# Performance work log

Measured on AMD Instinct MI355X. Metric: run time of the kernel, lower is better.

## Reference

```python
import jax, jax.numpy as jnp
import numpy as np

K, M, N = 8, 1024, 1024  # bits, in_features, out_features (nf)
B_, S_ = 4, 2048

def setup_inputs() -> dict:
    key = jax.random.key(0)
    k1, k2, k3, k4 = jax.random.split(key, 4)
    x = jax.random.normal(k1, (B_, S_, M), dtype=jnp.float32)
    # per-bit +/-1 sign matrices, stored as float (module casts int8 -> x.dtype)
    binary = jnp.where(jax.random.normal(k2, (K, M, N)) > 0, 1.0, -1.0).astype(jnp.float32)
    # positive per-bit, per-output-channel scales (sup decomposition yields positives)
    scale = jax.random.uniform(k3, (K, 1, N), dtype=jnp.float32, minval=0.01, maxval=1.0)
    bias = jax.random.normal(k4, (N,), dtype=jnp.float32)
    return {"x": x, "binary": binary, "scale": scale, "bias": bias}

def reference(x, binary, scale, bias):
    size_out = x.shape[:-1] + (N,)
    x2 = x.reshape(-1, x.shape[-1])                 # [T, m]
    # k separate dense matmuls against +/-1 matrices: [k, T, n]
    xk = jnp.einsum('tm,kmn->ktn', x2, binary)
    out = jnp.sum(xk * scale, axis=0)               # per-bit scale then sum over bits
    out = out + bias
    return out.reshape(size_out)
```

## Files before the change

kernel.cpp:

```cpp
#include <hip/hip_runtime.h>
#include <cstdint>

#define TDIM 8192
#define MDIM 1024
#define NDIM 1024
#define KBITS 8
#define BK 64

typedef __bf16 bf16x8 __attribute__((ext_vector_type(8)));
typedef float f32x4 __attribute__((ext_vector_type(4)));

#define GAS(p) ((__attribute__((address_space(1))) void*)(uintptr_t)(p))
#define LAS(p) ((__attribute__((address_space(3))) void*)(uintptr_t)(p))

__device__ __forceinline__ unsigned short f2bf(float f) {
    union { float f; unsigned u; } v; v.f = f;
    unsigned r = v.u + 0x7fffu + ((v.u >> 16) & 1u);
    return (unsigned short)(r >> 16);
}

__global__ __launch_bounds__(256) void prep_kernel(const float* __restrict__ x,
                                                   unsigned short* __restrict__ xb,
                                                   const float* __restrict__ binary,
                                                   const float* __restrict__ scale,
                                                   unsigned short* __restrict__ wtr) {
    __shared__ float tile[32][33];
    const int tid = threadIdx.x;
    if (blockIdx.x >= 1024) {
        size_t idx = ((size_t)(blockIdx.x - 1024) * 256 + tid) * 8;
        float4 a = *(const float4*)(x + idx);
        float4 b = *(const float4*)(x + idx + 4);
        uint4 o;
        o.x = (unsigned)f2bf(a.x) | ((unsigned)f2bf(a.y) << 16);
        o.y = (unsigned)f2bf(a.z) | ((unsigned)f2bf(a.w) << 16);
        o.z = (unsigned)f2bf(b.x) | ((unsigned)f2bf(b.y) << 16);
        o.w = (unsigned)f2bf(b.z) | ((unsigned)f2bf(b.w) << 16);
        *(uint4*)(xb + idx) = o;
        return;
    }
    const int n0 = (blockIdx.x & 31) * 32;
    const int m0 = (blockIdx.x >> 5) * 32;
    const int r = tid >> 3;
    const int cn = (tid & 7) * 4;
    f32x4 acc = {0.f, 0.f, 0.f, 0.f};
#pragma unroll
    for (int k = 0; k < KBITS; ++k) {
        f32x4 v = *(const f32x4*)(binary + ((size_t)k * MDIM + m0 + r) * NDIM + n0 + cn);
        f32x4 s = *(const f32x4*)(scale + (size_t)k * NDIM + n0 + cn);
        acc += v * s;
    }
#pragma unroll
    for (int e = 0; e < 4; ++e) tile[cn + e][r] = acc[e];
    __syncthreads();
    const int rn = tid >> 3;
    const int cm = (tid & 7) * 4;
    ushort4 o4;
    o4.x = f2bf(tile[rn][cm + 0]);
    o4.y = f2bf(tile[rn][cm + 1]);
    o4.z = f2bf(tile[rn][cm + 2]);
    o4.w = f2bf(tile[rn][cm + 3]);
    *(ushort4*)(wtr + (size_t)(n0 + rn) * MDIM + m0 + cm) = o4;
}

__global__ __launch_bounds__(256) void gemm_kernel(const unsigned short* __restrict__ xb,
                                                   const unsigned short* __restrict__ wtr,
                                                   const float* __restrict__ bias,
                                                   float* __restrict__ out) {
    __shared__ __attribute__((aligned(16))) unsigned short sA[128 * BK];
    __shared__ __attribute__((aligned(16))) unsigned short sB[128 * BK];

    const int tid = threadIdx.x;
    const int lane = tid & 63;
    const int wv = tid >> 6;
    const int wrow = wv >> 1;
    const int wcol = wv & 1;
    const int lrow = lane & 15;
    const int q = lane >> 4;

    const int t0 = blockIdx.x * 128;
    const int n0 = blockIdx.y * 128;

    const unsigned short* srcA[4];
    const unsigned short* srcB[4];
    unsigned short* dstA[4];
    unsigned short* dstB[4];
#pragma unroll
    for (int j = 0; j < 4; ++j) {
        int s = tid + j * 256;
        int r = s >> 3;
        int g = (s & 7) ^ (r & 7);
        srcA[j] = xb + (size_t)(t0 + r) * MDIM + g * 8;
        srcB[j] = wtr + (size_t)(n0 + r) * MDIM + g * 8;
        dstA[j] = sA + s * 8;
        dstB[j] = sB + s * 8;
    }

    int a_off[2][4], b_off[2][4];
#pragma unroll
    for (int h = 0; h < 2; ++h)
#pragma unroll
        for (int i = 0; i < 4; ++i) {
            int m = wrow * 64 + i * 16 + lrow;
            a_off[h][i] = (m * 8 + ((h * 4 + q) ^ (m & 7))) * 8;
            int n = wcol * 64 + i * 16 + lrow;
            b_off[h][i] = (n * 8 + ((h * 4 + q) ^ (n & 7))) * 8;
        }

    f32x4 acc[4][4];
    const f32x4 zero = {0.f, 0.f, 0.f, 0.f};
#pragma unroll
    for (int i = 0; i < 4; ++i)
#pragma unroll
        for (int j = 0; j < 4; ++j) acc[i][j] = zero;

    for (int k0 = 0; k0 < MDIM; k0 += BK) {
#pragma unroll
        for (int j = 0; j < 4; ++j)
            __builtin_amdgcn_global_load_lds(GAS(srcA[j] + k0), LAS(dstA[j]), 16, 0, 0);
#pragma unroll
        for (int j = 0; j < 4; ++j)
            __builtin_amdgcn_global_load_lds(GAS(srcB[j] + k0), LAS(dstB[j]), 16, 0, 0);
        __syncthreads();

#pragma unroll
        for (int h = 0; h < 2; ++h) {
            bf16x8 af[4], bfr[4];
#pragma unroll
            for (int i = 0; i < 4; ++i) af[i] = *(const bf16x8*)(sA + a_off[h][i]);
#pragma unroll
            for (int i = 0; i < 4; ++i) bfr[i] = *(const bf16x8*)(sB + b_off[h][i]);
#pragma unroll
            for (int i = 0; i < 4; ++i)
#pragma unroll
                for (int j = 0; j < 4; ++j)
                    acc[i][j] = __builtin_amdgcn_mfma_f32_16x16x32_bf16(af[i], bfr[j],
                                                                        acc[i][j], 0, 0, 0);
        }
        __syncthreads();
    }

#pragma unroll
    for (int j = 0; j < 4; ++j) {
        const int n = n0 + wcol * 64 + j * 16 + lrow;
        const float bv = bias[n];
#pragma unroll
        for (int i = 0; i < 4; ++i) {
            const int tb = t0 + wrow * 64 + i * 16 + q * 4;
#pragma unroll
            for (int r = 0; r < 4; ++r) {
                out[(size_t)(tb + r) * NDIM + n] = acc[i][j][r] + bv;
            }
        }
    }
}

extern "C" void kernel_launch(void* const* d_in, const int* in_sizes, int n_in,
                              void* d_out, int out_size, void* d_ws, size_t ws_size,
                              hipStream_t stream) {
    const float* x      = (const float*)d_in[0];
    const float* binary = (const float*)d_in[1];
    const float* scale  = (const float*)d_in[2];
    const float* bias   = (const float*)d_in[3];
    float* out = (float*)d_out;

    unsigned short* xb  = (unsigned short*)d_ws;
    unsigned short* wtr = xb + (size_t)TDIM * MDIM;

    prep_kernel<<<1024 + 4096, 256, 0, stream>>>(x, xb, binary, scale, wtr);
    gemm_kernel<<<dim3(TDIM / 128, NDIM / 128), 256, 0, stream>>>(xb, wtr, bias, out);
}
```

Baseline: 126.0 us.

## Triple-buffer LDS with 256x128 tiles and 512-thread blocks in GEMM

The GEMM moves from a single-buffered 128x128 tile with two barriers per K step to a 256x128 tile computed by 8 waves. A three-stage LDS ring issues global-to-LDS loads two tiles ahead and uses explicit vmcnt waits plus a single barrier per iteration. MFMA sections are also raised to higher priority with s_setprio. The aim is to hide global load latency and raise reuse of B per block, at the cost of about 144KB of LDS per block, which can cap occupancy at one block per CU and leaves fewer blocks (256) to fill the GPU.

```diff
diff --git a/kernel.cpp b/kernel.cpp
--- a/kernel.cpp
+++ b/kernel.cpp
@@ -6,6 +6,9 @@
 #define NDIM 1024
 #define KBITS 8
 #define BK 64
+#define BT 256
+#define BN 128
+#define NTILES (MDIM / BK)
 
 typedef __bf16 bf16x8 __attribute__((ext_vector_type(8)));
 typedef float f32x4 __attribute__((ext_vector_type(4)));
@@ -62,37 +65,45 @@
     *(ushort4*)(wtr + (size_t)(n0 + rn) * MDIM + m0 + cm) = o4;
 }
 
-__global__ __launch_bounds__(256) void gemm_kernel(const unsigned short* __restrict__ xb,
-                                                   const unsigned short* __restrict__ wtr,
-                                                   const float* __restrict__ bias,
-                                                   float* __restrict__ out) {
-    __shared__ __attribute__((aligned(16))) unsigned short sA[128 * BK];
-    __shared__ __attribute__((aligned(16))) unsigned short sB[128 * BK];
+__global__ __launch_bounds__(512, 2) void gemm_kernel(const unsigned short* __restrict__ xb,
+                                                      const unsigned short* __restrict__ wtr,
+                                                      const float* __restrict__ bias,
+                                                      float* __restrict__ out) {
+    constexpr int ASZ = BT * BK;
+    constexpr int BSZ = BN * BK;
+    constexpr int BUF = ASZ + BSZ;
+    __shared__ __attribute__((aligned(16))) unsigned short lds[3 * BUF];
 
     const int tid = threadIdx.x;
     const int lane = tid & 63;
     const int wv = tid >> 6;
-    const int wrow = wv >> 1;
-    const int wcol = wv & 1;
+    const int wm = wv >> 1;
+    const int wn = wv & 1;
     const int lrow = lane & 15;
     const int q = lane >> 4;
 
-    const int t0 = blockIdx.x * 128;
-    const int n0 = blockIdx.y * 128;
+    const int t0 = blockIdx.x * BT;
+    const int n0 = blockIdx.y * BN;
 
     const unsigned short* srcA[4];
-    const unsigned short* srcB[4];
-    unsigned short* dstA[4];
-    unsigned short* dstB[4];
+    int dstA[4];
+    const unsigned short* srcB[2];
+    int dstB[2];
 #pragma unroll
     for (int j = 0; j < 4; ++j) {
-        int s = tid + j * 256;
+        int s = tid + j * 512;
         int r = s >> 3;
         int g = (s & 7) ^ (r & 7);
         srcA[j] = xb + (size_t)(t0 + r) * MDIM + g * 8;
+        dstA[j] = s * 8;
+    }
+#pragma unroll
+    for (int j = 0; j < 2; ++j) {
+        int s = tid + j * 512;
+        int r = s >> 3;
+        int g = (s & 7) ^ (r & 7);
         srcB[j] = wtr + (size_t)(n0 + r) * MDIM + g * 8;
-        dstA[j] = sA + s * 8;
-        dstB[j] = sB + s * 8;
+        dstB[j] = ASZ + s * 8;
     }
 
     int a_off[2][4], b_off[2][4];
@@ -100,10 +111,10 @@
     for (int h = 0; h < 2; ++h)
 #pragma unroll
         for (int i = 0; i < 4; ++i) {
-            int m = wrow * 64 + i * 16 + lrow;
+            int m = wm * 64 + i * 16 + lrow;
             a_off[h][i] = (m * 8 + ((h * 4 + q) ^ (m & 7))) * 8;
-            int n = wcol * 64 + i * 16 + lrow;
-            b_off[h][i] = (n * 8 + ((h * 4 + q) ^ (n & 7))) * 8;
+            int n = wn * 64 + i * 16 + lrow;
+            b_off[h][i] = ASZ + (n * 8 + ((h * 4 + q) ^ (n & 7))) * 8;
         }
 
     f32x4 acc[4][4];
@@ -113,39 +124,64 @@
 #pragma unroll
         for (int j = 0; j < 4; ++j) acc[i][j] = zero;
 
-    for (int k0 = 0; k0 < MDIM; k0 += BK) {
+    auto stage = [&](int bufsel, int t) {
+        unsigned short* bb = lds + bufsel * BUF;
+        const int k0 = t * BK;
 #pragma unroll
         for (int j = 0; j < 4; ++j)
-            __builtin_amdgcn_global_load_lds(GAS(srcA[j] + k0), LAS(dstA[j]), 16, 0, 0);
-#pragma unroll
-        for (int j = 0; j < 4; ++j)
-            __builtin_amdgcn_global_load_lds(GAS(srcB[j] + k0), LAS(dstB[j]), 16, 0, 0);
-        __syncthreads();
-
+            __builtin_amdgcn_global_load_lds(GAS(srcA[j] + k0), LAS(bb + dstA[j]), 16, 0, 0);
+#pragma unroll
+        for (int j = 0; j < 2; ++j)
+            __builtin_amdgcn_global_load_lds(GAS(srcB[j] + k0), LAS(bb + dstB[j]), 16, 0, 0);
+    };
+
+    stage(0, 0);
+    stage(1, 1);
+    asm volatile("s_waitcnt vmcnt(6)" ::: "memory");
+    __builtin_amdgcn_s_barrier();
+    __builtin_amdgcn_sched_barrier(0);
+
+#pragma unroll
+    for (int t = 0; t < NTILES; ++t) {
+        const int cur = t % 3;
+        if (t + 2 < NTILES) stage((t + 2) % 3, t + 2);
+
+        const unsigned short* base = lds + cur * BUF;
 #pragma unroll
         for (int h = 0; h < 2; ++h) {
             bf16x8 af[4], bfr[4];
 #pragma unroll
-            for (int i = 0; i < 4; ++i) af[i] = *(const bf16x8*)(sA + a_off[h][i]);
-#pragma unroll
-            for (int i = 0; i < 4; ++i) bfr[i] = *(const bf16x8*)(sB + b_off[h][i]);
+            for (int i = 0; i < 4; ++i) af[i] = *(const bf16x8*)(base + a_off[h][i]);
+#pragma unroll
+            for (int i = 0; i < 4; ++i) bfr[i] = *(const bf16x8*)(base + b_off[h][i]);
+            __builtin_amdgcn_s_setprio(1);
 #pragma unroll
             for (int i = 0; i < 4; ++i)
 #pragma unroll
                 for (int j = 0; j < 4; ++j)
                     acc[i][j] = __builtin_amdgcn_mfma_f32_16x16x32_bf16(af[i], bfr[j],
                                                                         acc[i][j], 0, 0, 0);
-        }
-        __syncthreads();
+            __builtin_amdgcn_s_setprio(0);
+        }
+
+        if (t + 1 < NTILES) {
+            if (t + 2 < NTILES) {
+                asm volatile("s_waitcnt vmcnt(6)" ::: "memory");
+            } else {
+                asm volatile("s_waitcnt vmcnt(0)" ::: "memory");
+            }
+            __builtin_amdgcn_s_barrier();
+            __builtin_amdgcn_sched_barrier(0);
+        }
     }
 
 #pragma unroll
     for (int j = 0; j < 4; ++j) {
-        const int n = n0 + wcol * 64 + j * 16 + lrow;
+        const int n = n0 + wn * 64 + j * 16 + lrow;
         const float bv = bias[n];
 #pragma unroll
         for (int i = 0; i < 4; ++i) {
-            const int tb = t0 + wrow * 64 + i * 16 + q * 4;
+            const int tb = t0 + wm * 64 + i * 16 + q * 4;
 #pragma unroll
             for (int r = 0; r < 4; ++r) {
                 out[(size_t)(tb + r) * NDIM + n] = acc[i][j][r] + bv;
@@ -167,5 +203,5 @@
     unsigned short* wtr = xb + (size_t)TDIM * MDIM;
 
     prep_kernel<<<1024 + 4096, 256, 0, stream>>>(x, xb, binary, scale, wtr);
-    gemm_kernel<<<dim3(TDIM / 128, NDIM / 128), 256, 0, stream>>>(xb, wtr, bias, out);
-}
+    gemm_kernel<<<dim3(TDIM / BT, NDIM / BN), 512, 0, stream>>>(xb, wtr, bias, out);
+}
```

Measured after the change: 123.5 us. Within noise of the previous version (-2.0%).
